# Performance work log

Measured on AMD Instinct MI355X. Metric: run time of the kernel, lower is better.

The kernel has to match this reference:

```python
import jax, jax.numpy as jnp
import numpy as np
from jax.ops import segment_sum

N, E, D, P, F_IN, L, G = 40000, 320000, 128, 16, 64, 3, 40


def setup_inputs():
    key = jax.random.key(0)
    ks = iter(jax.random.split(key, 64))
    nrm = lambda shape, s=0.1: s * jax.random.normal(next(ks), shape, jnp.float32)
    inp = {
        "node_feat": nrm((N, F_IN), 1.0),
        "pos_enc": nrm((N, P), 1.0),
        "edge_feat": nrm((E, 1), 1.0),
        "snorm_n": jnp.full((N, 1), 1.0 / np.sqrt(N / G), jnp.float32),
        "edge_src": jax.random.randint(next(ks), (E,), 0, N, jnp.int32),
        "edge_dst": jax.random.randint(next(ks), (E,), 0, N, jnp.int32),
        "batch_num_nodes": jnp.full((G,), N // G, jnp.int32),
        "W_h": nrm((F_IN, D)), "b_h": jnp.zeros((D,), jnp.float32),
        "W_p": nrm((P, D)), "b_p": jnp.zeros((D,), jnp.float32),
        "W_e": nrm((1, D)), "b_e": jnp.zeros((D,), jnp.float32),
        "A1_W": nrm((L, 2 * D, D)), "A1_b": jnp.zeros((L, D), jnp.float32),
        "A2_W": nrm((L, 2 * D, D)), "A2_b": jnp.zeros((L, D), jnp.float32),
        "B1_W": nrm((L, D, D)), "B1_b": jnp.zeros((L, D), jnp.float32),
        "B2_W": nrm((L, D, D)), "B2_b": jnp.zeros((L, D), jnp.float32),
        "B3_W": nrm((L, D, D)), "B3_b": jnp.zeros((L, D), jnp.float32),
        "C1_W": nrm((L, D, D)), "C1_b": jnp.zeros((L, D), jnp.float32),
        "C2_W": nrm((L, D, D)), "C2_b": jnp.zeros((L, D), jnp.float32),
        "bn_h_g": jnp.ones((L, D), jnp.float32), "bn_h_b": jnp.zeros((L, D), jnp.float32),
        "bn_e_g": jnp.ones((L, D), jnp.float32), "bn_e_b": jnp.zeros((L, D), jnp.float32),
        "pout_W": nrm((D, P)), "pout_b": jnp.zeros((P,), jnp.float32),
        "Whp_W": nrm((D + P, D)), "Whp_b": jnp.zeros((D,), jnp.float32),
        "mlp_W0": nrm((D, D // 2)), "mlp_b0": jnp.zeros((D // 2,), jnp.float32),
        "mlp_W1": nrm((D // 2, D // 4)), "mlp_b1": jnp.zeros((D // 4,), jnp.float32),
        "mlp_W2": nrm((D // 4, 1)), "mlp_b2": jnp.zeros((1,), jnp.float32),
    }
    return inp


def _bn(x, g, b, eps=1e-5):
    # BatchNorm1d with batch statistics (training-mode math, eval dropout)
    m = x.mean(0)
    v = x.var(0)
    return g * (x - m) / jnp.sqrt(v + eps) + b


def _forward(fl, edge_src, edge_dst, batch_num_nodes):
    n = fl["node_feat"].shape[0]
    h = fl["node_feat"] @ fl["W_h"] + fl["b_h"]
    p = fl["pos_enc"] @ fl["W_p"] + fl["b_p"]
    e = fl["edge_feat"] @ fl["W_e"] + fl["b_e"]
    snorm = fl["snorm_n"]
    for l in range(L):
        h_in, p_in, e_in = h, p, e
        hp_cat = jnp.concatenate([h, p], -1)                      # [N, 2D]
        A1h = hp_cat @ fl["A1_W"][l] + fl["A1_b"][l]
        A2h = hp_cat @ fl["A2_W"][l] + fl["A2_b"][l]
        B1h = h @ fl["B1_W"][l] + fl["B1_b"][l]
        B2h = h @ fl["B2_W"][l] + fl["B2_b"][l]
        B3e = e @ fl["B3_W"][l] + fl["B3_b"][l]
        hat_eta = B1h[edge_src] + B2h[edge_dst] + B3e             # [E, D]
        sigma = jax.nn.sigmoid(hat_eta)
        ssum = segment_sum(sigma, edge_dst, num_segments=n)       # [N, D]
        eta = sigma / (ssum[edge_dst] + 1e-6)                     # [E, D]
        h_new = A1h + segment_sum(eta * A2h[edge_src], edge_dst, num_segments=n)
        C1p = p @ fl["C1_W"][l] + fl["C1_b"][l]
        C2p = p @ fl["C2_W"][l] + fl["C2_b"][l]
        p_new = C1p + segment_sum(eta * C2p[edge_src], edge_dst, num_segments=n)
        h2 = jax.nn.relu(_bn(h_new * snorm, fl["bn_h_g"][l], fl["bn_h_b"][l]))
        e2 = jax.nn.relu(_bn(hat_eta, fl["bn_e_g"][l], fl["bn_e_b"][l]))
        p2 = jnp.tanh(p_new)
        h, p, e = h_in + h2, p_in + p2, e_in + e2                 # residual
    # LSPE readout: per-graph center and per-feature L2-normalize p
    p = p @ fl["pout_W"] + fl["pout_b"]                           # [N, P]
    gid = jnp.repeat(jnp.arange(G), batch_num_nodes, total_repeat_length=n)
    cnt = batch_num_nodes.astype(p.dtype)[:, None]
    p = p - (segment_sum(p, gid, num_segments=G) / cnt)[gid]
    p = p / jnp.sqrt(segment_sum(p * p, gid, num_segments=G))[gid]
    hp = jnp.concatenate([h, p], -1) @ fl["Whp_W"] + fl["Whp_b"]
    first_idx = jnp.concatenate([jnp.zeros((1,), jnp.int32),
                                 jnp.cumsum(batch_num_nodes)[:-1].astype(jnp.int32)])
    hg = hp[first_idx]                                            # [G, D]
    y = jax.nn.relu(hg @ fl["mlp_W0"] + fl["mlp_b0"])
    y = jax.nn.relu(y @ fl["mlp_W1"] + fl["mlp_b1"])
    return y @ fl["mlp_W2"] + fl["mlp_b2"]                        # [G, 1]


def reference(node_feat, pos_enc, edge_feat, snorm_n, edge_src, edge_dst,
              batch_num_nodes, W_h, b_h, W_p, b_p, W_e, b_e,
              A1_W, A1_b, A2_W, A2_b, B1_W, B1_b, B2_W, B2_b, B3_W, B3_b,
              C1_W, C1_b, C2_W, C2_b, bn_h_g, bn_h_b, bn_e_g, bn_e_b,
              pout_W, pout_b, Whp_W, Whp_b,
              mlp_W0, mlp_b0, mlp_W1, mlp_b1, mlp_W2, mlp_b2):
    args = dict(locals())
    src = args.pop("edge_src")
    dst = args.pop("edge_dst")
    bnn = args.pop("batch_num_nodes")
    return _forward(args, src, dst, bnn)
```

## Files before the change

kernel.cpp:

```cpp
#include <hip/hip_runtime.h>

#define NN 40000
#define NNP 40064
#define NE 320000
#define DD 128
#define PP 16
#define FIN 64
#define NL 3
#define NG 40

typedef float4 f4;
typedef __attribute__((ext_vector_type(4))) float f32x4;
typedef _Float16 hf;
typedef __attribute__((ext_vector_type(4))) _Float16 h4;
typedef __attribute__((ext_vector_type(8))) _Float16 h8;

__device__ hf    g_e   [NE * DD];
__device__ hf    g_heta[NE * DD];
__device__ float g_h   [NNP * DD], g_p [NNP * DD];
__device__ hf    g_h16 [NNP * DD], g_pf [NNP * DD];
__device__ float g_A1h [NNP * DD], g_C1p[NNP * DD];
__device__ hf    g_A2h [NNP * DD], g_B1h[NNP * DD], g_B2h[NNP * DD], g_C2p[NNP * DD];
__device__ float g_st  [768];
__device__ float g_p16 [NN * PP], g_psum[NG * PP], g_pss[NG * PP];
__device__ int   g_cum [64];
__device__ int   g_deg[NN], g_rowptr[NN + 1], g_cursor[NN], g_perm[NE], g_ssrc[NE], g_sdst[NE];
__device__ hf    g_WA[2 * NL * DD * 256];
__device__ hf    g_WB[5 * NL * DD * DD];

__device__ __forceinline__ float sigm(float x) { return 1.0f / (1.0f + __expf(-x)); }

__global__ void k_zero(float* __restrict__ p, int n4)
{
    int i = blockIdx.x * 256 + threadIdx.x;
    if (i < n4) ((f4*)p)[i] = f4{0.f, 0.f, 0.f, 0.f};
}

__global__ void k_zeroi(int* __restrict__ p, int n)
{
    int i = blockIdx.x * 256 + threadIdx.x;
    if (i < n) p[i] = 0;
}

__global__ void k_deg(const int* __restrict__ dst, int* __restrict__ deg)
{
    int e = blockIdx.x * 256 + threadIdx.x;
    if (e < NE) atomicAdd(&deg[dst[e]], 1);
}

__global__ __launch_bounds__(1024)
void k_scan(const int* __restrict__ deg, int* __restrict__ rowptr, int* __restrict__ cursor)
{
    __shared__ int sums[1024];
    int t = threadIdx.x;
    const int chunk = (NN + 1023) / 1024;
    int base = t * chunk;
    int s = 0;
    for (int i = 0; i < chunk; ++i) { int idx = base + i; if (idx < NN) s += deg[idx]; }
    sums[t] = s;
    __syncthreads();
    for (int off = 1; off < 1024; off <<= 1) {
        int v = (t >= off) ? sums[t - off] : 0;
        __syncthreads();
        sums[t] += v;
        __syncthreads();
    }
    int run = (t == 0) ? 0 : sums[t - 1];
    for (int i = 0; i < chunk; ++i) {
        int idx = base + i;
        if (idx < NN) { rowptr[idx] = run; cursor[idx] = run; run += deg[idx]; }
    }
    if (t == 1023) rowptr[NN] = sums[1023];
}

__global__ void k_fill(const int* __restrict__ dst, int* __restrict__ cursor,
                       int* __restrict__ perm)
{
    int e = blockIdx.x * 256 + threadIdx.x;
    if (e < NE) {
        int pos = atomicAdd(&cursor[dst[e]], 1);
        perm[pos] = e;
    }
}

__global__ void k_sortidx(const int* __restrict__ perm, const int* __restrict__ src,
                          const int* __restrict__ dst, int* __restrict__ ssrc,
                          int* __restrict__ sdst)
{
    int i = blockIdx.x * 256 + threadIdx.x;
    if (i < NE) { int e = perm[i]; ssrc[i] = src[e]; sdst[i] = dst[e]; }
}

__global__ void k_wprepA(const float* __restrict__ A1W, const float* __restrict__ A2W,
                         hf* __restrict__ outh)
{
    int which = blockIdx.z, l = blockIdx.y;
    int idx = blockIdx.x * 256 + threadIdx.x;
    int k = idx >> 7, n = idx & 127;
    const float* W = (which == 0 ? A1W : A2W) + (size_t)l * 256 * 128;
    outh[((size_t)which * NL + l) * DD * 256 + (size_t)n * 256 + k] = (hf)W[k * 128 + n];
}

__global__ void k_wprepB(const float* __restrict__ B1W, const float* __restrict__ B2W,
                         const float* __restrict__ B3W, const float* __restrict__ C1W,
                         const float* __restrict__ C2W, hf* __restrict__ outh)
{
    int which = blockIdx.z, l = blockIdx.y;
    int idx = blockIdx.x * 256 + threadIdx.x;
    int k = idx >> 7, n = idx & 127;
    const float* W;
    switch (which) { case 0: W = B1W; break; case 1: W = B2W; break;
                     case 2: W = B3W; break; case 3: W = C1W; break; default: W = C2W; }
    W += (size_t)l * 128 * 128;
    outh[((size_t)which * NL + l) * DD * DD + (size_t)n * 128 + k] = (hf)W[k * 128 + n];
}

template<int K>
__global__ __launch_bounds__(256)
void k_gemmF(const float* __restrict__ A, const float* __restrict__ W,
             const float* __restrict__ bias, float* __restrict__ C)
{
    __shared__ float As[64][20];
    __shared__ float Ws[16][128];
    const int tid = threadIdx.x;
    const int m0 = blockIdx.x * 64;
    const int ti = tid >> 4;
    const int tj = tid & 15;
    float acc[4][8];
    {
        float bv[8];
        #pragma unroll
        for (int c = 0; c < 8; ++c) bv[c] = bias[tj * 8 + c];
        #pragma unroll
        for (int r = 0; r < 4; ++r)
            #pragma unroll
            for (int c = 0; c < 8; ++c) acc[r][c] = bv[c];
    }
    const int ar = tid >> 2;
    const int ac = (tid & 3) * 4;
    for (int k0 = 0; k0 < K; k0 += 16) {
        f4 av = *(const f4*)(A + (size_t)(m0 + ar) * K + k0 + ac);
        *(f4*)&As[ar][ac] = av;
        {
            int q = tid;   int kr = q >> 5, c4 = (q & 31) * 4;
            *(f4*)&Ws[kr][c4] = *(const f4*)(W + (size_t)(k0 + kr) * 128 + c4);
            q = tid + 256; kr = q >> 5; c4 = (q & 31) * 4;
            *(f4*)&Ws[kr][c4] = *(const f4*)(W + (size_t)(k0 + kr) * 128 + c4);
        }
        __syncthreads();
        #pragma unroll
        for (int kk = 0; kk < 16; ++kk) {
            float a0 = As[ti * 4 + 0][kk];
            float a1 = As[ti * 4 + 1][kk];
            float a2 = As[ti * 4 + 2][kk];
            float a3 = As[ti * 4 + 3][kk];
            f4 w0 = *(f4*)&Ws[kk][tj * 8];
            f4 w1 = *(f4*)&Ws[kk][tj * 8 + 4];
            float wv[8] = {w0.x, w0.y, w0.z, w0.w, w1.x, w1.y, w1.z, w1.w};
            #pragma unroll
            for (int c = 0; c < 8; ++c) {
                acc[0][c] += a0 * wv[c];
                acc[1][c] += a1 * wv[c];
                acc[2][c] += a2 * wv[c];
                acc[3][c] += a3 * wv[c];
            }
        }
        __syncthreads();
    }
    #pragma unroll
    for (int r = 0; r < 4; ++r) {
        int row = m0 + ti * 4 + r;
        f4 o0 = {acc[r][0], acc[r][1], acc[r][2], acc[r][3]};
        f4 o1 = {acc[r][4], acc[r][5], acc[r][6], acc[r][7]};
        *(f4*)(C + (size_t)row * 128 + tj * 8)     = o0;
        *(f4*)(C + (size_t)row * 128 + tj * 8 + 4) = o1;
    }
}

struct NArgs {
    const hf* W[6];
    const float* bs[6];
    void* out[6];
};

__global__ __launch_bounds__(256)
void k_gemmN(NArgs a, const hf* __restrict__ hp, const hf* __restrict__ pp)
{
    __shared__ __align__(16) char smem[20480];
    hf (*As)[40] = (hf(*)[40])smem;
    hf (*Wh)[40] = (hf(*)[40])(smem + 10240);
    float* fstg = (float*)smem;
    hf*    hstg = (hf*)smem;
    const int tid = threadIdx.x;
    const int y = blockIdx.y;
    const int m0 = blockIdx.x * 128;
    const int K = (y < 2) ? 256 : 128;
    const hf* Wt = a.W[y];
    const int wid = tid >> 6, lane = tid & 63;
    const int lg = lane >> 4, ln = lane & 15;

    f32x4 acc[2][8];
    #pragma unroll
    for (int mt = 0; mt < 2; ++mt)
        #pragma unroll
        for (int nt = 0; nt < 8; ++nt) acc[mt][nt] = f32x4{0.f, 0.f, 0.f, 0.f};

    const int r1 = tid >> 2, g1 = (tid & 3) * 8;
    const int r2 = r1 + 64,  g2 = g1;

    for (int k0 = 0; k0 < K; k0 += 32) {
        const hf* pA; int kk;
        if (y < 2) {
            if (k0 >= 128) { pA = pp; kk = k0 - 128; }
            else           { pA = hp; kk = k0; }
        } else if (y < 4) { pA = hp; kk = k0; }
        else              { pA = pp; kk = k0; }
        *(f4*)&As[r1][g1] = *(const f4*)(pA + (size_t)(m0 + r1) * 128 + kk + g1);
        *(f4*)&As[r2][g2] = *(const f4*)(pA + (size_t)(m0 + r2) * 128 + kk + g2);
        *(f4*)&Wh[r1][g1] = *(const f4*)(Wt + (size_t)r1 * K + k0 + g1);
        *(f4*)&Wh[r2][g2] = *(const f4*)(Wt + (size_t)r2 * K + k0 + g2);
        __syncthreads();

        const int koff = lg * 8;
        h8 a0 = *(h8*)&As[wid * 32 + ln][koff];
        h8 a1 = *(h8*)&As[wid * 32 + 16 + ln][koff];
        #pragma unroll
        for (int nt = 0; nt < 8; ++nt) {
            h8 wh = *(h8*)&Wh[nt * 16 + ln][koff];
            acc[0][nt] = __builtin_amdgcn_mfma_f32_16x16x32_f16(a0, wh, acc[0][nt], 0, 0, 0);
            acc[1][nt] = __builtin_amdgcn_mfma_f32_16x16x32_f16(a1, wh, acc[1][nt], 0, 0, 0);
        }
        __syncthreads();
    }

    const float* bias = a.bs[y];
    const bool isF32 = (y == 0 || y == 4);
    if (isF32) {
        float* C = (float*)a.out[y];
        for (int pass = 0; pass < 4; ++pass) {
            if (wid == pass) {
                #pragma unroll
                for (int mt = 0; mt < 2; ++mt)
                    #pragma unroll
                    for (int nt = 0; nt < 8; ++nt)
                        #pragma unroll
                        for (int j = 0; j < 4; ++j)
                            fstg[(mt * 16 + lg * 4 + j) * 132 + nt * 16 + ln]
                                = acc[mt][nt][j] + bias[nt * 16 + ln];
            }
            __syncthreads();
            #pragma unroll
            for (int it = 0; it < 4; ++it) {
                int idx = it * 256 + tid;
                int r = idx >> 5, c4 = (idx & 31) * 4;
                *(f4*)(C + (size_t)(m0 + pass * 32 + r) * 128 + c4) = *(f4*)&fstg[r * 132 + c4];
            }
            __syncthreads();
        }
    } else {
        hf* C = (hf*)a.out[y];
        for (int pass = 0; pass < 4; ++pass) {
            if (wid == pass) {
                #pragma unroll
                for (int mt = 0; mt < 2; ++mt)
                    #pragma unroll
                    for (int nt = 0; nt < 8; ++nt)
                        #pragma unroll
                        for (int j = 0; j < 4; ++j)
                            hstg[(mt * 16 + lg * 4 + j) * 136 + nt * 16 + ln]
                                = (hf)(acc[mt][nt][j] + bias[nt * 16 + ln]);
            }
            __syncthreads();
            #pragma unroll
            for (int it = 0; it < 2; ++it) {
                int idx = it * 256 + tid;
                int r = idx >> 4, c8 = (idx & 15) * 8;
                *(f4*)(C + (size_t)(m0 + pass * 32 + r) * 128 + c8) = *(f4*)&hstg[r * 136 + c8];
            }
            __syncthreads();
        }
    }
}

template<bool EUPD, bool STATS>
__global__ __launch_bounds__(256)
void k_gemmE(hf* E, const hf* hetaPrev, hf* Cheta,
             const float* __restrict__ estPrev, const float* __restrict__ gamE,
             const float* __restrict__ betE,
             const hf* __restrict__ Wt,
             const float* __restrict__ bias,
             const hf* __restrict__ Gs, const hf* __restrict__ Gd,
             const int* __restrict__ srcI, const int* __restrict__ dstI,
             float* st, int wb)
{
    __shared__ __align__(16) char smem[20480];
    __shared__ float bnS[128], bnT[128];
    hf (*Ae)[40] = (hf(*)[40])smem;
    hf (*Wh)[40] = (hf(*)[40])(smem + 10240);
    float* sred = (float*)smem;
    hf*    hstg = (hf*)(smem + 1024);
    const int tid = threadIdx.x;
    const int m0 = blockIdx.x * 128;
    const int wid = tid >> 6, lane = tid & 63;
    const int lg = lane >> 4, ln = lane & 15;

    if (EUPD) {
        if (tid < 128) {
            const float invME = 1.0f / NE;
            float m = estPrev[tid] * invME;
            float v = estPrev[128 + tid] * invME - m * m;
            float inv = 1.0f / sqrtf(v + 1e-5f);
            float gg = gamE[tid];
            bnS[tid] = gg * inv;
            bnT[tid] = betE[tid] - gg * m * inv;
        }
        __syncthreads();
    }

    f32x4 acc[2][8];
    #pragma unroll
    for (int mt = 0; mt < 2; ++mt)
        #pragma unroll
        for (int nt = 0; nt < 8; ++nt) acc[mt][nt] = f32x4{0.f, 0.f, 0.f, 0.f};

    const int r1 = tid >> 2, g1 = (tid & 3) * 8;
    const int r2 = r1 + 64,  g2 = g1;

    for (int k0 = 0; k0 < 128; k0 += 32) {
        if (EUPD) {
            #pragma unroll
            for (int half = 0; half < 2; ++half) {
                int r = half ? r2 : r1;
                int g = half ? g2 : g1;
                int row = m0 + r, cb = k0 + g;
                h8 ev = *(const h8*)(E + (size_t)row * 128 + cb);
                h8 tv = *(const h8*)(hetaPrev + (size_t)row * 128 + cb);
                h8 nv;
                #pragma unroll
                for (int j = 0; j < 8; ++j) {
                    float xn = (float)tv[j] * bnS[cb + j] + bnT[cb + j];
                    float en = (float)ev[j] + fmaxf(xn, 0.f);
                    nv[j] = (hf)en;
                }
                *(h8*)&Ae[r][g] = nv;
                if (wb) *(h8*)(E + (size_t)row * 128 + cb) = nv;
            }
        } else {
            *(f4*)&Ae[r1][g1] = *(const f4*)(E + (size_t)(m0 + r1) * 128 + k0 + g1);
            *(f4*)&Ae[r2][g2] = *(const f4*)(E + (size_t)(m0 + r2) * 128 + k0 + g2);
        }
        *(f4*)&Wh[r1][g1] = *(const f4*)(Wt + (size_t)r1 * 128 + k0 + g1);
        *(f4*)&Wh[r2][g2] = *(const f4*)(Wt + (size_t)r2 * 128 + k0 + g2);
        __syncthreads();

        const int koff = lg * 8;
        h8 a0 = *(h8*)&Ae[wid * 32 + ln][koff];
        h8 a1 = *(h8*)&Ae[wid * 32 + 16 + ln][koff];
        #pragma unroll
        for (int nt = 0; nt < 8; ++nt) {
            h8 wh = *(h8*)&Wh[nt * 16 + ln][koff];
            acc[0][nt] = __builtin_amdgcn_mfma_f32_16x16x32_f16(a0, wh, acc[0][nt], 0, 0, 0);
            acc[1][nt] = __builtin_amdgcn_mfma_f32_16x16x32_f16(a1, wh, acc[1][nt], 0, 0, 0);
        }
        __syncthreads();
    }

    if (STATS) { sred[tid] = 0.f; __syncthreads(); }

    #pragma unroll
    for (int mt = 0; mt < 2; ++mt) {
        const int grow = m0 + wid * 32 + mt * 16 + lg * 4;
        int sa[4], da[4];
        #pragma unroll
        for (int j = 0; j < 4; ++j) { sa[j] = srcI[grow + j]; da[j] = dstI[grow + j]; }
        #pragma unroll
        for (int nt = 0; nt < 8; ++nt) {
            const int col = nt * 16 + ln;
            const float b = bias[col];
            float ls = 0.f, lq = 0.f;
            #pragma unroll
            for (int j = 0; j < 4; ++j) {
                float x = acc[mt][nt][j] + b
                        + (float)Gs[(size_t)sa[j] * 128 + col]
                        + (float)Gd[(size_t)da[j] * 128 + col];
                acc[mt][nt][j] = x;
                if (STATS) { ls += x; lq += x * x; }
            }
            if (STATS) {
                ls += __shfl_xor(ls, 16); ls += __shfl_xor(ls, 32);
                lq += __shfl_xor(lq, 16); lq += __shfl_xor(lq, 32);
                if (lane < 16) {
                    atomicAdd(&sred[col], ls);
                    atomicAdd(&sred[128 + col], lq);
                }
            }
        }
    }

    for (int pass = 0; pass < 4; ++pass) {
        if (wid == pass) {
            #pragma unroll
            for (int mt = 0; mt < 2; ++mt)
                #pragma unroll
                for (int nt = 0; nt < 8; ++nt)
                    #pragma unroll
                    for (int j = 0; j < 4; ++j)
                        hstg[(mt * 16 + lg * 4 + j) * 136 + nt * 16 + ln]
                            = (hf)acc[mt][nt][j];
        }
        __syncthreads();
        #pragma unroll
        for (int it = 0; it < 2; ++it) {
            int idx = it * 256 + tid;
            int r = idx >> 4, c8 = (idx & 15) * 8;
            *(f4*)(Cheta + (size_t)(m0 + pass * 32 + r) * 128 + c8) = *(f4*)&hstg[r * 136 + c8];
        }
        __syncthreads();
    }
    if (STATS) atomicAdd(&st[tid], sred[tid]);
}


__global__ void k_cvt16(const float* __restrict__ x, hf* __restrict__ y, int n4)
{
    int i = blockIdx.x * 256 + threadIdx.x;
    if (i >= n4) return;
    f4 v = ((const f4*)x)[i];
    ((h4*)y)[i] = h4{(hf)v.x, (hf)v.y, (hf)v.z, (hf)v.w};
}

__global__ void k_einit(const float* __restrict__ ef, const int* __restrict__ perm,
                        const float* __restrict__ We, const float* __restrict__ be,
                        hf* __restrict__ E)
{
    size_t id = (size_t)blockIdx.x * 256 + threadIdx.x;
    int row = (int)(id >> 5);
    int c = (int)(id & 31) * 4;
    float s = ef[perm[row]];
    f4 w = *(const f4*)(We + c);
    f4 b = *(const f4*)(be + c);
    *(h4*)(E + (size_t)row * 128 + c)
        = h4{(hf)(s * w.x + b.x), (hf)(s * w.y + b.y), (hf)(s * w.z + b.z), (hf)(s * w.w + b.w)};
}

__global__ void k_agg(const hf* __restrict__ heta, const hf* __restrict__ A2h,
                      const hf* __restrict__ C2p, const int* __restrict__ rowptr,
                      const int* __restrict__ ssrc, const float* __restrict__ snorm,
                      float* __restrict__ A1h, const float* __restrict__ C1p,
                      float* __restrict__ p, hf* __restrict__ pf,
                      float* __restrict__ st, int wp)
{
    int id = blockIdx.x * 256 + threadIdx.x;
    int row = id >> 4;
    int c = (id & 15) * 8;

    int s0 = rowptr[row], s1 = rowptr[row + 1];

    float ss[8], ah[8], cp[8];
    #pragma unroll
    for (int j = 0; j < 8; ++j) { ss[j] = 0.f; ah[j] = 0.f; cp[j] = 0.f; }

    int e = s0;
    for (; e + 1 < s1; e += 2) {
        int sA = ssrc[e], sB = ssrc[e + 1];
        h8 vA = *(const h8*)(heta + (size_t)e * 128 + c);
        h8 vB = *(const h8*)(heta + (size_t)(e + 1) * 128 + c);
        h8 aA = *(const h8*)(A2h + (size_t)sA * 128 + c);
        h8 aB = *(const h8*)(A2h + (size_t)sB * 128 + c);
        h8 cA = *(const h8*)(C2p + (size_t)sA * 128 + c);
        h8 cB = *(const h8*)(C2p + (size_t)sB * 128 + c);
        #pragma unroll
        for (int j = 0; j < 8; ++j) {
            float gA = sigm((float)vA[j]);
            float gB = sigm((float)vB[j]);
            ss[j] += gA + gB;
            ah[j] += gA * (float)aA[j] + gB * (float)aB[j];
            cp[j] += gA * (float)cA[j] + gB * (float)cB[j];
        }
    }
    if (e < s1) {
        int sA = ssrc[e];
        h8 vA = *(const h8*)(heta + (size_t)e * 128 + c);
        h8 aA = *(const h8*)(A2h + (size_t)sA * 128 + c);
        h8 cA = *(const h8*)(C2p + (size_t)sA * 128 + c);
        #pragma unroll
        for (int j = 0; j < 8; ++j) {
            float gA = sigm((float)vA[j]);
            ss[j] += gA;
            ah[j] += gA * (float)aA[j];
            cp[j] += gA * (float)cA[j];
        }
    }

    float hx[8];
    {
        float sn = snorm[row];
        f4 a1lo = *(const f4*)(A1h + (size_t)row * 128 + c);
        f4 a1hi = *(const f4*)(A1h + (size_t)row * 128 + c + 4);
        float a1[8] = {a1lo.x, a1lo.y, a1lo.z, a1lo.w, a1hi.x, a1hi.y, a1hi.z, a1hi.w};
        #pragma unroll
        for (int j = 0; j < 8; ++j) {
            float d = ss[j] + 1e-6f;
            hx[j] = (a1[j] + ah[j] / d) * sn;
            cp[j] = cp[j] / d;
        }
        f4 o0 = {hx[0], hx[1], hx[2], hx[3]};
        f4 o1 = {hx[4], hx[5], hx[6], hx[7]};
        *(f4*)(A1h + (size_t)row * 128 + c)     = o0;
        *(f4*)(A1h + (size_t)row * 128 + c + 4) = o1;
    }

    {
        f4 c1lo = *(const f4*)(C1p + (size_t)row * 128 + c);
        f4 c1hi = *(const f4*)(C1p + (size_t)row * 128 + c + 4);
        float c1[8] = {c1lo.x, c1lo.y, c1lo.z, c1lo.w, c1hi.x, c1hi.y, c1hi.z, c1hi.w};
        f4 pvlo = *(const f4*)(p + (size_t)row * 128 + c);
        f4 pvhi = *(const f4*)(p + (size_t)row * 128 + c + 4);
        float pv[8] = {pvlo.x, pvlo.y, pvlo.z, pvlo.w, pvhi.x, pvhi.y, pvhi.z, pvhi.w};
        #pragma unroll
        for (int j = 0; j < 8; ++j) pv[j] += tanhf(c1[j] + cp[j]);
        f4 o0 = {pv[0], pv[1], pv[2], pv[3]};
        f4 o1 = {pv[4], pv[5], pv[6], pv[7]};
        *(f4*)(p + (size_t)row * 128 + c)     = o0;
        *(f4*)(p + (size_t)row * 128 + c + 4) = o1;
        if (wp) {
            h8 ph;
            #pragma unroll
            for (int j = 0; j < 8; ++j) ph[j] = (hf)pv[j];
            *(h8*)(pf + (size_t)row * 128 + c) = ph;
        }
    }

    __shared__ float red[16][128];
    int lrow = threadIdx.x >> 4;
    #pragma unroll
    for (int j = 0; j < 8; ++j) red[lrow][c + j] = hx[j];
    __syncthreads();
    if (threadIdx.x < 128) {
        float a = 0.f;
        #pragma unroll
        for (int q = 0; q < 16; ++q) a += red[q][threadIdx.x];
        atomicAdd(&st[threadIdx.x], a);
    }
    __syncthreads();
    #pragma unroll
    for (int j = 0; j < 8; ++j) red[lrow][c + j] = hx[j] * hx[j];
    __syncthreads();
    if (threadIdx.x < 128) {
        float a = 0.f;
        #pragma unroll
        for (int q = 0; q < 16; ++q) a += red[q][threadIdx.x];
        atomicAdd(&st[128 + threadIdx.x], a);
    }
}

__global__ void k_bnupd_h(float* __restrict__ Y, hf* __restrict__ Y16,
                          const float* __restrict__ X, const float* __restrict__ st,
                          const float* __restrict__ gam, const float* __restrict__ bet, float invM)
{
    size_t id = (size_t)blockIdx.x * 256 + threadIdx.x;
    int row = (int)(id >> 5);
    int c = (int)(id & 31) * 4;
    f4 x  = *(const f4*)(X + (size_t)row * 128 + c);
    f4 s  = *(const f4*)(st + c);
    f4 s2 = *(const f4*)(st + 128 + c);
    f4 g  = *(const f4*)(gam + c);
    f4 b  = *(const f4*)(bet + c);
    f4 y  = *(const f4*)(Y + (size_t)row * 128 + c);
    float m, v, o;
    m = s.x * invM; v = s2.x * invM - m * m; o = g.x * (x.x - m) / sqrtf(v + 1e-5f) + b.x; y.x += fmaxf(o, 0.f);
    m = s.y * invM; v = s2.y * invM - m * m; o = g.y * (x.y - m) / sqrtf(v + 1e-5f) + b.y; y.y += fmaxf(o, 0.f);
    m = s.z * invM; v = s2.z * invM - m * m; o = g.z * (x.z - m) / sqrtf(v + 1e-5f) + b.z; y.z += fmaxf(o, 0.f);
    m = s.w * invM; v = s2.w * invM - m * m; o = g.w * (x.w - m) / sqrtf(v + 1e-5f) + b.w; y.w += fmaxf(o, 0.f);
    *(f4*)(Y + (size_t)row * 128 + c) = y;
    *(h4*)(Y16 + (size_t)row * 128 + c) = h4{(hf)y.x, (hf)y.y, (hf)y.z, (hf)y.w};
}


__global__ void k_p16(const float* __restrict__ p, const float* __restrict__ poutW,
                      const float* __restrict__ poutb, float* __restrict__ p16)
{
    int id = blockIdx.x * 256 + threadIdx.x;
    int i = id >> 4, c = id & 15;
    float a = poutb[c];
    for (int k = 0; k < 128; ++k) a += p[(size_t)i * 128 + k] * poutW[k * 16 + c];
    p16[id] = a;
}

__global__ void k_cum(const int* __restrict__ bnn, int* __restrict__ cum)
{
    if (threadIdx.x == 0) {
        cum[0] = 0;
        for (int g = 0; g < NG; ++g) cum[g + 1] = cum[g] + bnn[g];
    }
}

__global__ void k_graphstats(const float* __restrict__ p16, const int* __restrict__ cum,
                             float* __restrict__ psum, float* __restrict__ pss)
{
    int g = blockIdx.x;
    int t = threadIdx.x;
    int c = t & 15, s = t >> 4;
    int start = cum[g], end = cum[g + 1];
    float cnt = (float)(end - start);
    __shared__ float red[16][17];
    __shared__ float meanv[16];
    float loc = 0.f;
    for (int i = start + s; i < end; i += 16) loc += p16[(size_t)i * 16 + c];
    red[s][c] = loc;
    __syncthreads();
    if (s == 0) {
        float a = 0.f;
        #pragma unroll
        for (int q = 0; q < 16; ++q) a += red[q][c];
        psum[g * 16 + c] = a;
        meanv[c] = a / cnt;
    }
    __syncthreads();
    float m = meanv[c];
    loc = 0.f;
    for (int i = start + s; i < end; i += 16) {
        float v = p16[(size_t)i * 16 + c] - m;
        loc += v * v;
    }
    red[s][c] = loc;
    __syncthreads();
    if (s == 0) {
        float a = 0.f;
        #pragma unroll
        for (int q = 0; q < 16; ++q) a += red[q][c];
        pss[g * 16 + c] = a;
    }
}

__global__ void k_final(const float* __restrict__ h, const float* __restrict__ A1h,
                        const float* __restrict__ hst, const float* __restrict__ gam,
                        const float* __restrict__ bet,
                        const float* __restrict__ p16,
                        const float* __restrict__ psum, const float* __restrict__ pss,
                        const int* __restrict__ cum,
                        const float* __restrict__ WhpW, const float* __restrict__ Whpb,
                        const float* __restrict__ W0, const float* __restrict__ b0,
                        const float* __restrict__ W1, const float* __restrict__ b1,
                        const float* __restrict__ W2, const float* __restrict__ b2,
                        float* __restrict__ out)
{
    int g = blockIdx.x;
    int t = threadIdx.x;
    __shared__ float hpc[144];
    __shared__ float hpv[128];
    __shared__ float y0[64];
    __shared__ float y1[32];
    int fi = cum[g];
    float cnt = (float)(cum[g + 1] - cum[g]);
    {
        const float invM = 1.0f / NN;
        float m = hst[t] * invM;
        float v = hst[128 + t] * invM - m * m;
        float x = A1h[(size_t)fi * 128 + t];
        float o = gam[t] * (x - m) / sqrtf(v + 1e-5f) + bet[t];
        hpc[t] = h[(size_t)fi * 128 + t] + fmaxf(o, 0.f);
    }
    if (t < 16) {
        float centered = p16[(size_t)fi * 16 + t] - psum[g * 16 + t] / cnt;
        hpc[128 + t] = centered / sqrtf(pss[g * 16 + t]);
    }
    __syncthreads();
    float acc = Whpb[t];
    for (int k = 0; k < 144; ++k) acc += hpc[k] * WhpW[k * 128 + t];
    hpv[t] = acc;
    __syncthreads();
    if (t < 64) {
        float a = b0[t];
        for (int k = 0; k < 128; ++k) a += hpv[k] * W0[k * 64 + t];
        y0[t] = fmaxf(a, 0.f);
    }
    __syncthreads();
    if (t < 32) {
        float a = b1[t];
        for (int k = 0; k < 64; ++k) a += y0[k] * W1[k * 32 + t];
        y1[t] = fmaxf(a, 0.f);
    }
    __syncthreads();
    if (t == 0) {
        float a = b2[0];
        for (int k = 0; k < 32; ++k) a += y1[k] * W2[k];
        out[g] = a;
    }
}


extern "C" void kernel_launch(void* const* d_in, const int* in_sizes, int n_in,
                              void* d_out, int out_size, void* d_ws, size_t ws_size,
                              hipStream_t stream)
{
    (void)in_sizes; (void)n_in; (void)out_size; (void)d_ws; (void)ws_size;
    const float* node_feat = (const float*)d_in[0];
    const float* pos_enc   = (const float*)d_in[1];
    const float* edge_feat = (const float*)d_in[2];
    const float* snorm     = (const float*)d_in[3];
    const int*   src       = (const int*)d_in[4];
    const int*   dst       = (const int*)d_in[5];
    const int*   bnn       = (const int*)d_in[6];
    const float* W_h = (const float*)d_in[7],  *b_h = (const float*)d_in[8];
    const float* W_p = (const float*)d_in[9],  *b_p = (const float*)d_in[10];
    const float* W_e = (const float*)d_in[11], *b_e = (const float*)d_in[12];
    const float* A1W = (const float*)d_in[13], *A1b = (const float*)d_in[14];
    const float* A2W = (const float*)d_in[15], *A2b = (const float*)d_in[16];
    const float* B1W = (const float*)d_in[17], *B1b = (const float*)d_in[18];
    const float* B2W = (const float*)d_in[19], *B2b = (const float*)d_in[20];
    const float* B3W = (const float*)d_in[21], *B3b = (const float*)d_in[22];
    const float* C1W = (const float*)d_in[23], *C1b = (const float*)d_in[24];
    const float* C2W = (const float*)d_in[25], *C2b = (const float*)d_in[26];
    const float* bnhg = (const float*)d_in[27], *bnhb = (const float*)d_in[28];
    const float* bneg = (const float*)d_in[29], *bneb = (const float*)d_in[30];
    const float* poutW = (const float*)d_in[31], *poutb = (const float*)d_in[32];
    const float* WhpW = (const float*)d_in[33], *Whpb = (const float*)d_in[34];
    const float* W0 = (const float*)d_in[35], *b0 = (const float*)d_in[36];
    const float* W1 = (const float*)d_in[37], *b1 = (const float*)d_in[38];
    const float* W2 = (const float*)d_in[39], *b2 = (const float*)d_in[40];
    float* out = (float*)d_out;

    float *h, *p, *A1h, *C1p, *st, *p16, *psum, *pss;
    hf *e, *heta, *h16, *pf, *A2h, *B1h, *B2h, *C2p, *WA, *WB;
    int *cum, *deg, *rowptr, *cursor, *perm, *ssrc, *sdst;
    hipGetSymbolAddress((void**)&e,      HIP_SYMBOL(g_e));
    hipGetSymbolAddress((void**)&heta,   HIP_SYMBOL(g_heta));
    hipGetSymbolAddress((void**)&h,      HIP_SYMBOL(g_h));
    hipGetSymbolAddress((void**)&p,      HIP_SYMBOL(g_p));
    hipGetSymbolAddress((void**)&h16,    HIP_SYMBOL(g_h16));
    hipGetSymbolAddress((void**)&pf,     HIP_SYMBOL(g_pf));
    hipGetSymbolAddress((void**)&A1h,    HIP_SYMBOL(g_A1h));
    hipGetSymbolAddress((void**)&C1p,    HIP_SYMBOL(g_C1p));
    hipGetSymbolAddress((void**)&A2h,    HIP_SYMBOL(g_A2h));
    hipGetSymbolAddress((void**)&B1h,    HIP_SYMBOL(g_B1h));
    hipGetSymbolAddress((void**)&B2h,    HIP_SYMBOL(g_B2h));
    hipGetSymbolAddress((void**)&C2p,    HIP_SYMBOL(g_C2p));
    hipGetSymbolAddress((void**)&st,     HIP_SYMBOL(g_st));
    hipGetSymbolAddress((void**)&p16,    HIP_SYMBOL(g_p16));
    hipGetSymbolAddress((void**)&psum,   HIP_SYMBOL(g_psum));
    hipGetSymbolAddress((void**)&pss,    HIP_SYMBOL(g_pss));
    hipGetSymbolAddress((void**)&cum,    HIP_SYMBOL(g_cum));
    hipGetSymbolAddress((void**)&deg,    HIP_SYMBOL(g_deg));
    hipGetSymbolAddress((void**)&rowptr, HIP_SYMBOL(g_rowptr));
    hipGetSymbolAddress((void**)&cursor, HIP_SYMBOL(g_cursor));
    hipGetSymbolAddress((void**)&perm,   HIP_SYMBOL(g_perm));
    hipGetSymbolAddress((void**)&ssrc,   HIP_SYMBOL(g_ssrc));
    hipGetSymbolAddress((void**)&sdst,   HIP_SYMBOL(g_sdst));
    hipGetSymbolAddress((void**)&WA,     HIP_SYMBOL(g_WA));
    hipGetSymbolAddress((void**)&WB,     HIP_SYMBOL(g_WB));
    float* hst  = st;
    float* estA = st + 256;
    float* estB = st + 512;

    k_zeroi<<<(NN + 255) / 256, 256, 0, stream>>>(deg, NN);
    k_deg<<<(NE + 255) / 256, 256, 0, stream>>>(dst, deg);
    k_scan<<<1, 1024, 0, stream>>>(deg, rowptr, cursor);
    k_fill<<<(NE + 255) / 256, 256, 0, stream>>>(dst, cursor, perm);
    k_sortidx<<<(NE + 255) / 256, 256, 0, stream>>>(perm, src, dst, ssrc, sdst);
    k_wprepA<<<dim3(128, NL, 2), 256, 0, stream>>>(A1W, A2W, WA);
    k_wprepB<<<dim3(64, NL, 5), 256, 0, stream>>>(B1W, B2W, B3W, C1W, C2W, WB);

    k_gemmF<FIN><<<NN / 64, 256, 0, stream>>>(node_feat, W_h, b_h, h);
    k_gemmF<PP ><<<NN / 64, 256, 0, stream>>>(pos_enc,  W_p, b_p, p);
    k_cvt16<<<(NNP * 32 + 255) / 256, 256, 0, stream>>>(h, h16, NNP * 32);
    k_cvt16<<<(NNP * 32 + 255) / 256, 256, 0, stream>>>(p, pf, NNP * 32);
    k_einit<<<NE * 32 / 256, 256, 0, stream>>>(edge_feat, perm, W_e, b_e, e);

    const int NB = NNP / 128;
    for (int l = 0; l < NL; ++l) {
        const hf* WB3 = WB + (size_t)(2 * NL + l) * DD * DD;

        NArgs na;
        na.W[0] = WA + (size_t)(0 * NL + l) * DD * 256;
        na.W[1] = WA + (size_t)(1 * NL + l) * DD * 256;
        na.W[2] = WB + (size_t)(0 * NL + l) * DD * DD;
        na.W[3] = WB + (size_t)(1 * NL + l) * DD * DD;
        na.W[4] = WB + (size_t)(3 * NL + l) * DD * DD;
        na.W[5] = WB + (size_t)(4 * NL + l) * DD * DD;
        na.bs[0] = A1b + l * DD; na.bs[1] = A2b + l * DD;
        na.bs[2] = B1b + l * DD; na.bs[3] = B2b + l * DD;
        na.bs[4] = C1b + l * DD; na.bs[5] = C2b + l * DD;
        na.out[0] = A1h; na.out[1] = A2h; na.out[2] = B1h;
        na.out[3] = B2h; na.out[4] = C1p; na.out[5] = C2p;
        k_gemmN<<<dim3(NB, 6), 256, 0, stream>>>(na, h16, pf);

        k_zero<<<1, 256, 0, stream>>>(hst, 64);

        if (l == 0) {
            k_zero<<<1, 256, 0, stream>>>(estA, 64);
            k_gemmE<false, true><<<NE / 128, 256, 0, stream>>>(
                e, nullptr, heta, nullptr, nullptr, nullptr,
                WB3, B3b + l * DD, B1h, B2h, ssrc, sdst, estA, 0);
        } else if (l == 1) {
            k_zero<<<1, 256, 0, stream>>>(estB, 64);
            k_gemmE<true, true><<<NE / 128, 256, 0, stream>>>(
                e, heta, heta, estA, bneg + 0 * DD, bneb + 0 * DD,
                WB3, B3b + l * DD, B1h, B2h, ssrc, sdst, estB, 1);
        } else {
            k_gemmE<true, false><<<NE / 128, 256, 0, stream>>>(
                e, heta, heta, estB, bneg + 1 * DD, bneb + 1 * DD,
                WB3, B3b + l * DD, B1h, B2h, ssrc, sdst, nullptr, 0);
        }

        k_agg<<<NN * 16 / 256, 256, 0, stream>>>(heta, A2h, C2p, rowptr, ssrc, snorm,
                                                 A1h, C1p, p, pf, hst,
                                                 (l < NL - 1) ? 1 : 0);

        if (l < NL - 1)
            k_bnupd_h<<<NN * 32 / 256, 256, 0, stream>>>(h, h16, A1h, hst,
                                                         bnhg + l * DD, bnhb + l * DD, 1.0f / NN);
    }

    k_p16<<<NN * 16 / 256, 256, 0, stream>>>(p, poutW, poutb, p16);
    k_cum<<<1, 64, 0, stream>>>(bnn, cum);
    k_graphstats<<<NG, 256, 0, stream>>>(p16, cum, psum, pss);
    k_final<<<NG, 128, 0, stream>>>(h, A1h, hst, bnhg + (NL - 1) * DD, bnhb + (NL - 1) * DD,
                                    p16, psum, pss, cum,
                                    WhpW, Whpb, W0, b0, W1, b1, W2, b2, out);
}
```

Baseline: 1.065 ms.

## Split edge GEMM across two column-half blocks with ping-pong edge buffers

The edge GEMM grid gains a second dimension, so each block computes 64 of the 128 output columns and there are twice as many smaller blocks. Because both column halves read the full input row, in-place updates of e and heta would race, so separate ping-pong buffers are added for e and heta. Only the first column block writes back the updated e. The aim is more parallelism and lower register and LDS use per block, at the cost of recomputing the BN/ReLU update of the A tile in both halves and re-reading the edge inputs twice.

```diff
diff --git a/kernel.cpp b/kernel.cpp
--- a/kernel.cpp
+++ b/kernel.cpp
@@ -15,8 +15,8 @@
 typedef __attribute__((ext_vector_type(4))) _Float16 h4;
 typedef __attribute__((ext_vector_type(8))) _Float16 h8;
 
-__device__ hf    g_e   [NE * DD];
-__device__ hf    g_heta[NE * DD];
+__device__ hf    g_e   [NE * DD], g_e2[NE * DD];
+__device__ hf    g_heta[NE * DD], g_heta2[NE * DD];
 __device__ float g_h   [NNP * DD], g_p [NNP * DD];
 __device__ hf    g_h16 [NNP * DD], g_pf [NNP * DD];
 __device__ float g_A1h [NNP * DD], g_C1p[NNP * DD];
@@ -284,7 +284,7 @@
 
 template<bool EUPD, bool STATS>
 __global__ __launch_bounds__(256)
-void k_gemmE(hf* E, const hf* hetaPrev, hf* Cheta,
+void k_gemmE(const hf* Ein, hf* Eout, const hf* hetaPrev, hf* Cheta,
              const float* __restrict__ estPrev, const float* __restrict__ gamE,
              const float* __restrict__ betE,
              const hf* __restrict__ Wt,
@@ -293,7 +293,7 @@
              const int* __restrict__ srcI, const int* __restrict__ dstI,
              float* st, int wb)
 {
-    __shared__ __align__(16) char smem[20480];
+    __shared__ __align__(16) char smem[15360];
     __shared__ float bnS[128], bnT[128];
     hf (*Ae)[40] = (hf(*)[40])smem;
     hf (*Wh)[40] = (hf(*)[40])(smem + 10240);
@@ -301,6 +301,7 @@
     hf*    hstg = (hf*)(smem + 1024);
     const int tid = threadIdx.x;
     const int m0 = blockIdx.x * 128;
+    const int nc0 = blockIdx.y * 64;
     const int wid = tid >> 6, lane = tid & 63;
     const int lg = lane >> 4, ln = lane & 15;
 
@@ -317,14 +318,18 @@
         __syncthreads();
     }
 
-    f32x4 acc[2][8];
+    f32x4 acc[2][4];
     #pragma unroll
     for (int mt = 0; mt < 2; ++mt)
         #pragma unroll
-        for (int nt = 0; nt < 8; ++nt) acc[mt][nt] = f32x4{0.f, 0.f, 0.f, 0.f};
+        for (int nt = 0; nt < 4; ++nt) acc[mt][nt] = f32x4{0.f, 0.f, 0.f, 0.f};
 
     const int r1 = tid >> 2, g1 = (tid & 3) * 8;
     const int r2 = r1 + 64,  g2 = g1;
+    const int wr = tid >> 2;
+    const int wg = (tid & 3) * 8;
+
+    const bool doWb = (blockIdx.y == 0);
 
     for (int k0 = 0; k0 < 128; k0 += 32) {
         if (EUPD) {
@@ -333,7 +338,7 @@
                 int r = half ? r2 : r1;
                 int g = half ? g2 : g1;
                 int row = m0 + r, cb = k0 + g;
-                h8 ev = *(const h8*)(E + (size_t)row * 128 + cb);
+                h8 ev = *(const h8*)(Ein + (size_t)row * 128 + cb);
                 h8 tv = *(const h8*)(hetaPrev + (size_t)row * 128 + cb);
                 h8 nv;
                 #pragma unroll
@@ -343,21 +348,20 @@
                     nv[j] = (hf)en;
                 }
                 *(h8*)&Ae[r][g] = nv;
-                if (wb) *(h8*)(E + (size_t)row * 128 + cb) = nv;
+                if (wb && doWb) *(h8*)(Eout + (size_t)row * 128 + cb) = nv;
             }
         } else {
-            *(f4*)&Ae[r1][g1] = *(const f4*)(E + (size_t)(m0 + r1) * 128 + k0 + g1);
-            *(f4*)&Ae[r2][g2] = *(const f4*)(E + (size_t)(m0 + r2) * 128 + k0 + g2);
-        }
-        *(f4*)&Wh[r1][g1] = *(const f4*)(Wt + (size_t)r1 * 128 + k0 + g1);
-        *(f4*)&Wh[r2][g2] = *(const f4*)(Wt + (size_t)r2 * 128 + k0 + g2);
+            *(f4*)&Ae[r1][g1] = *(const f4*)(Ein + (size_t)(m0 + r1) * 128 + k0 + g1);
+            *(f4*)&Ae[r2][g2] = *(const f4*)(Ein + (size_t)(m0 + r2) * 128 + k0 + g2);
+        }
+        *(f4*)&Wh[wr][wg] = *(const f4*)(Wt + (size_t)(nc0 + wr) * 128 + k0 + wg);
         __syncthreads();
 
         const int koff = lg * 8;
         h8 a0 = *(h8*)&Ae[wid * 32 + ln][koff];
         h8 a1 = *(h8*)&Ae[wid * 32 + 16 + ln][koff];
         #pragma unroll
-        for (int nt = 0; nt < 8; ++nt) {
+        for (int nt = 0; nt < 4; ++nt) {
             h8 wh = *(h8*)&Wh[nt * 16 + ln][koff];
             acc[0][nt] = __builtin_amdgcn_mfma_f32_16x16x32_f16(a0, wh, acc[0][nt], 0, 0, 0);
             acc[1][nt] = __builtin_amdgcn_mfma_f32_16x16x32_f16(a1, wh, acc[1][nt], 0, 0, 0);
@@ -374,8 +378,8 @@
         #pragma unroll
         for (int j = 0; j < 4; ++j) { sa[j] = srcI[grow + j]; da[j] = dstI[grow + j]; }
         #pragma unroll
-        for (int nt = 0; nt < 8; ++nt) {
-            const int col = nt * 16 + ln;
+        for (int nt = 0; nt < 4; ++nt) {
+            const int col = nc0 + nt * 16 + ln;
             const float b = bias[col];
             float ls = 0.f, lq = 0.f;
             #pragma unroll
@@ -402,18 +406,17 @@
             #pragma unroll
             for (int mt = 0; mt < 2; ++mt)
                 #pragma unroll
-                for (int nt = 0; nt < 8; ++nt)
+                for (int nt = 0; nt < 4; ++nt)
                     #pragma unroll
                     for (int j = 0; j < 4; ++j)
-                        hstg[(mt * 16 + lg * 4 + j) * 136 + nt * 16 + ln]
+                        hstg[(mt * 16 + lg * 4 + j) * 72 + nt * 16 + ln]
                             = (hf)acc[mt][nt][j];
         }
         __syncthreads();
-        #pragma unroll
-        for (int it = 0; it < 2; ++it) {
-            int idx = it * 256 + tid;
-            int r = idx >> 4, c8 = (idx & 15) * 8;
-            *(f4*)(Cheta + (size_t)(m0 + pass * 32 + r) * 128 + c8) = *(f4*)&hstg[r * 136 + c8];
+        {
+            int r = tid >> 3, c8 = (tid & 7) * 8;
+            *(f4*)(Cheta + (size_t)(m0 + pass * 32 + r) * 128 + nc0 + c8)
+                = *(f4*)&hstg[r * 72 + c8];
         }
         __syncthreads();
     }
@@ -722,10 +725,12 @@
     float* out = (float*)d_out;
 
     float *h, *p, *A1h, *C1p, *st, *p16, *psum, *pss;
-    hf *e, *heta, *h16, *pf, *A2h, *B1h, *B2h, *C2p, *WA, *WB;
+    hf *e, *e2, *het0, *het1, *h16, *pf, *A2h, *B1h, *B2h, *C2p, *WA, *WB;
     int *cum, *deg, *rowptr, *cursor, *perm, *ssrc, *sdst;
     hipGetSymbolAddress((void**)&e,      HIP_SYMBOL(g_e));
-    hipGetSymbolAddress((void**)&heta,   HIP_SYMBOL(g_heta));
+    hipGetSymbolAddress((void**)&e2,     HIP_SYMBOL(g_e2));
+    hipGetSymbolAddress((void**)&het0,   HIP_SYMBOL(g_heta));
+    hipGetSymbolAddress((void**)&het1,   HIP_SYMBOL(g_heta2));
     hipGetSymbolAddress((void**)&h,      HIP_SYMBOL(g_h));
     hipGetSymbolAddress((void**)&p,      HIP_SYMBOL(g_p));
     hipGetSymbolAddress((void**)&h16,    HIP_SYMBOL(g_h16));
@@ -787,23 +792,27 @@
 
         k_zero<<<1, 256, 0, stream>>>(hst, 64);
 
+        const hf* hetaL;
         if (l == 0) {
             k_zero<<<1, 256, 0, stream>>>(estA, 64);
-            k_gemmE<false, true><<<NE / 128, 256, 0, stream>>>(
-                e, nullptr, heta, nullptr, nullptr, nullptr,
+            k_gemmE<false, true><<<dim3(NE / 128, 2), 256, 0, stream>>>(
+                e, nullptr, nullptr, het0, nullptr, nullptr, nullptr,
                 WB3, B3b + l * DD, B1h, B2h, ssrc, sdst, estA, 0);
+            hetaL = het0;
         } else if (l == 1) {
             k_zero<<<1, 256, 0, stream>>>(estB, 64);
-            k_gemmE<true, true><<<NE / 128, 256, 0, stream>>>(
-                e, heta, heta, estA, bneg + 0 * DD, bneb + 0 * DD,
+            k_gemmE<true, true><<<dim3(NE / 128, 2), 256, 0, stream>>>(
+                e, e2, het0, het1, estA, bneg + 0 * DD, bneb + 0 * DD,
                 WB3, B3b + l * DD, B1h, B2h, ssrc, sdst, estB, 1);
+            hetaL = het1;
         } else {
-            k_gemmE<true, false><<<NE / 128, 256, 0, stream>>>(
-                e, heta, heta, estB, bneg + 1 * DD, bneb + 1 * DD,
+            k_gemmE<true, false><<<dim3(NE / 128, 2), 256, 0, stream>>>(
+                e2, nullptr, het1, het0, estB, bneg + 1 * DD, bneb + 1 * DD,
                 WB3, B3b + l * DD, B1h, B2h, ssrc, sdst, nullptr, 0);
-        }
-
-        k_agg<<<NN * 16 / 256, 256, 0, stream>>>(heta, A2h, C2p, rowptr, ssrc, snorm,
+            hetaL = het0;
+        }
+
+        k_agg<<<NN * 16 / 256, 256, 0, stream>>>(hetaL, A2h, C2p, rowptr, ssrc, snorm,
                                                  A1h, C1p, p, pf, hst,
                                                  (l < NL - 1) ? 1 : 0);
 
```

Result: slower. 1.564 ms (+46.9%).
